# Optimization experiments

Hardware: AMD Instinct MI355X
Metric: run time of the kernel (lower is better)

The kernel has to match this reference:

```python
import jax, jax.numpy as jnp
import numpy as np

NUM_HEADS = 32
NUM_KV_HEADS = 8
HEAD_DIM = 128
HIDDEN = 4096
EPS = 1e-6
ROPE_BASE = 10000.0
NEG_INF = -1e9


def setup_inputs() -> dict:
    key = jax.random.key(0)
    ks = jax.random.split(key, 6)
    B, S = 1, 2048
    hidden_states = jax.random.normal(ks[0], (B, S, HIDDEN), dtype=jnp.float32)
    wq = jax.random.normal(ks[1], (HIDDEN, NUM_HEADS * HEAD_DIM), dtype=jnp.float32) * 0.02
    wk = jax.random.normal(ks[2], (HIDDEN, NUM_KV_HEADS * HEAD_DIM), dtype=jnp.float32) * 0.02
    wv = jax.random.normal(ks[3], (HIDDEN, NUM_KV_HEADS * HEAD_DIM), dtype=jnp.float32) * 0.02
    wo = jax.random.normal(ks[4], (NUM_HEADS * HEAD_DIM, HIDDEN), dtype=jnp.float32) * 0.02
    q_norm_w = jnp.ones((HEAD_DIM,), dtype=jnp.float32)
    k_norm_w = jnp.ones((HEAD_DIM,), dtype=jnp.float32)
    attention_mask = jnp.tril(jnp.ones((S, S), dtype=bool))[None, None]  # [1,1,S,S] causal allow-mask
    position_ids = jnp.arange(S, dtype=jnp.int64 if jax.config.jax_enable_x64 else jnp.int32)[None, :]
    return dict(hidden_states=hidden_states, wq=wq, wk=wk, wv=wv, wo=wo,
                q_norm_w=q_norm_w, k_norm_w=k_norm_w,
                attention_mask=attention_mask, position_ids=position_ids)


def _rotate_half(x):
    x1, x2 = jnp.split(x, 2, axis=-1)
    return jnp.concatenate((-x2, x1), axis=-1)


def _rms_norm(x, w):
    xf = x.astype(jnp.float32)
    var = jnp.mean(xf * xf, axis=-1, keepdims=True)
    return w * (xf * jax.lax.rsqrt(var + EPS)).astype(x.dtype)


def reference(hidden_states, wq, wk, wv, wo, q_norm_w, k_norm_w, attention_mask, position_ids):
    B, S, _ = hidden_states.shape
    dtype = hidden_states.dtype

    # projections -> [B, H, S, D]
    q = (hidden_states @ wq).reshape(B, S, NUM_HEADS, HEAD_DIM).transpose(0, 2, 1, 3)
    k = (hidden_states @ wk).reshape(B, S, NUM_KV_HEADS, HEAD_DIM).transpose(0, 2, 1, 3)
    v = (hidden_states @ wv).reshape(B, S, NUM_KV_HEADS, HEAD_DIM).transpose(0, 2, 1, 3)

    # RoPE cache (fp32), gathered by position_ids
    inv_freq = 1.0 / (ROPE_BASE ** (jnp.arange(0, HEAD_DIM, 2, dtype=jnp.float32) / HEAD_DIM))
    t = jnp.arange(S, dtype=jnp.float32)
    freqs = jnp.outer(t, inv_freq)                    # [S, D/2]
    emb = jnp.concatenate((freqs, freqs), axis=-1)    # [S, D]
    cos = jnp.cos(emb).astype(dtype)[position_ids][:, None]  # [B,1,S,D]
    sin = jnp.sin(emb).astype(dtype)[position_ids][:, None]

    q = q * cos + _rotate_half(q) * sin
    k = k * cos + _rotate_half(k) * sin

    # QK RMSNorm (after RoPE)
    q = _rms_norm(q, q_norm_w)
    k = _rms_norm(k, k_norm_w)

    # GQA repeat-kv
    n_rep = NUM_HEADS // NUM_KV_HEADS
    k = jnp.repeat(k, n_rep, axis=1)
    v = jnp.repeat(v, n_rep, axis=1)

    scores = jnp.einsum('bhqd,bhkd->bhqk', q, k) / np.sqrt(HEAD_DIM)
    scores = jnp.where(attention_mask, scores, scores + NEG_INF)
    probs = jax.nn.softmax(scores.astype(jnp.float32), axis=-1).astype(dtype)
    out = jnp.einsum('bhqk,bhkd->bhqd', probs, v)      # [B,H,S,D]
    out = out.transpose(0, 2, 1, 3).reshape(B, S, NUM_HEADS * HEAD_DIM)
    return out @ wo
```

## Files before the change

kernel.cpp:

```cpp
#include <hip/hip_runtime.h>

typedef __bf16 bf16x8 __attribute__((ext_vector_type(8)));
typedef float f32x4 __attribute__((ext_vector_type(4)));
typedef unsigned short u16x8 __attribute__((ext_vector_type(8)));
typedef unsigned short u16x4 __attribute__((ext_vector_type(4)));
typedef unsigned short u16x2 __attribute__((ext_vector_type(2)));

__device__ inline unsigned short f2bf(float f) {
    return __builtin_bit_cast(unsigned short, (__bf16)f);
}
__device__ inline float bf2f(unsigned short u) {
    return (float)__builtin_bit_cast(__bf16, u);
}

__device__ inline void storeC(float v, float* p) { *p = v; }
__device__ inline void storeC(float v, unsigned short* p) { *p = f2bf(v); }

#define MFMA16(a, b, c) __builtin_amdgcn_mfma_f32_16x16x32_bf16( \
    __builtin_bit_cast(bf16x8, a), __builtin_bit_cast(bf16x8, b), (c), 0, 0, 0)

__device__ inline void gload16(const unsigned short* g, unsigned short* l) {
    __builtin_amdgcn_global_load_lds(
        (const __attribute__((address_space(1))) unsigned int*)(g),
        (__attribute__((address_space(3))) unsigned int*)(l), 16, 0, 0);
}

__device__ __forceinline__ void bar() {
    asm volatile("" ::: "memory");
    __builtin_amdgcn_s_barrier();
    asm volatile("" ::: "memory");
}
#define WAITVM(N) asm volatile("s_waitcnt vmcnt(" #N ")" ::: "memory")

__global__ __launch_bounds__(256) void convert_f32_bf16_swz(
    const float* __restrict__ X, unsigned short* __restrict__ Y)
{
    const size_t i = ((size_t)blockIdx.x * 256 + threadIdx.x) * 8;
    const size_t row7 = (i >> 12) & 7;
    float4 v0 = *(const float4*)&X[i];
    float4 v1 = *(const float4*)&X[i + 4];
    u16x8 o;
    o[0] = f2bf(v0.x); o[1] = f2bf(v0.y); o[2] = f2bf(v0.z); o[3] = f2bf(v0.w);
    o[4] = f2bf(v1.x); o[5] = f2bf(v1.y); o[6] = f2bf(v1.z); o[7] = f2bf(v1.w);
    *(u16x8*)&Y[i ^ (row7 << 3)] = o;
}

__global__ __launch_bounds__(256) void transpose_f32_bf16(
    const float* __restrict__ W, unsigned short* __restrict__ WT, int K, int N)
{
    constexpr int LDT = 66;
    __shared__ unsigned short t_lds[64 * LDT];
    const int kt = blockIdx.x * 64, nt = blockIdx.y * 64;
    const int tid = threadIdx.x;
    const int c = (tid & 15) * 4;
    #pragma unroll
    for (int p = 0; p < 4; ++p) {
        const int r = p * 16 + (tid >> 4);
        float4 v = *(const float4*)&W[(size_t)(kt + r) * N + nt + c];
        u16x2 h0, h1;
        h0[0] = f2bf(v.x); h0[1] = f2bf(v.y);
        h1[0] = f2bf(v.z); h1[1] = f2bf(v.w);
        *(u16x2*)&t_lds[r * LDT + c] = h0;
        *(u16x2*)&t_lds[r * LDT + c + 2] = h1;
    }
    __syncthreads();
    const int kc = (tid & 7) * 8;
    #pragma unroll
    for (int p = 0; p < 2; ++p) {
        const int n = p * 32 + (tid >> 3);
        u16x8 o;
        #pragma unroll
        for (int j = 0; j < 8; ++j) o[j] = t_lds[(kc + j) * LDT + n];
        *(u16x8*)&WT[(size_t)(nt + n) * K + kt + (kc ^ ((n & 7) << 3))] = o;
    }
}

template <typename CT, int CMODE>
__global__ __launch_bounds__(512) void gemm8(
    const unsigned short* __restrict__ A, const unsigned short* __restrict__ B,
    CT* __restrict__ C, CT* __restrict__ C2, int M, int N, int K)
{
    constexpr int ASZ = 128 * 64, BSZ = 256 * 64;
    __shared__ __attribute__((aligned(16))) unsigned short a_lds[3 * ASZ];
    __shared__ __attribute__((aligned(16))) unsigned short b_lds[3 * BSZ];

    const int bm0 = blockIdx.y * 128, bn0 = blockIdx.x * 256;
    const int tid = threadIdx.x, lane = tid & 63, wid = tid >> 6;
    const int wr = wid >> 2, wc = wid & 3;
    const int l15 = lane & 15, koff = (lane >> 4) * 8;
    const int sw = (l15 & 7) << 3;
    const int cb0 = koff ^ sw;
    const int cb1 = (32 + koff) ^ sw;

    f32x4 acc[4][4] = {};

    const unsigned short* ag[2];
    const unsigned short* bg[4];
    #pragma unroll
    for (int p = 0; p < 2; ++p) {
        const int row = (wid + p * 8) * 8 + (lane >> 3);
        ag[p] = A + (size_t)(bm0 + row) * K + (lane & 7) * 8;
    }
    #pragma unroll
    for (int p = 0; p < 4; ++p) {
        const int row = (wid + p * 8) * 8 + (lane >> 3);
        bg[p] = B + (size_t)(bn0 + row) * K + (lane & 7) * 8;
    }

    const int nt = K >> 6;

    auto stageA = [&](int s, int kt, int p) {
        gload16(ag[p] + kt, a_lds + s * ASZ + (wid + p * 8) * 512);
    };
    auto stageB = [&](int s, int kt, int p) {
        gload16(bg[p] + kt, b_lds + s * BSZ + (wid + p * 8) * 512);
    };

    #pragma unroll
    for (int p = 0; p < 2; ++p) stageA(0, 0, p);
    #pragma unroll
    for (int p = 0; p < 4; ++p) stageB(0, 0, p);
    #pragma unroll
    for (int p = 0; p < 2; ++p) stageA(1, 64, p);
    #pragma unroll
    for (int p = 0; p < 4; ++p) stageB(1, 64, p);
    WAITVM(6);
    bar();

    int sc = 0;
    for (int t = 0; t < nt; ++t) {
        const unsigned short* ab = a_lds + sc * ASZ;
        const unsigned short* bb = b_lds + sc * BSZ;
        const int ss = (sc >= 1) ? sc - 1 : 2;
        const int kt2 = (t + 2) << 6;
        const bool st = (t + 2) < nt;

        u16x8 af0, af1, af2, af3, bfr[4];

        af0 = *(const u16x8*)&ab[(wr * 64 + 0 * 16 + l15) * 64 + cb0];
        af1 = *(const u16x8*)&ab[(wr * 64 + 1 * 16 + l15) * 64 + cb0];
        af2 = *(const u16x8*)&ab[(wr * 64 + 2 * 16 + l15) * 64 + cb0];
        af3 = *(const u16x8*)&ab[(wr * 64 + 3 * 16 + l15) * 64 + cb0];
        #pragma unroll
        for (int j = 0; j < 4; ++j)
            bfr[j] = *(const u16x8*)&bb[(wc * 64 + j * 16 + l15) * 64 + cb0];
        if (st) { stageA(ss, kt2, 0); stageA(ss, kt2, 1); stageB(ss, kt2, 0); }
        bar();
        __builtin_amdgcn_s_setprio(1);
        #pragma unroll
        for (int j = 0; j < 4; ++j) {
            acc[0][j] = MFMA16(af0, bfr[j], acc[0][j]);
            acc[1][j] = MFMA16(af1, bfr[j], acc[1][j]);
            acc[2][j] = MFMA16(af2, bfr[j], acc[2][j]);
            acc[3][j] = MFMA16(af3, bfr[j], acc[3][j]);
        }
        __builtin_amdgcn_s_setprio(0);

        af0 = *(const u16x8*)&ab[(wr * 64 + 0 * 16 + l15) * 64 + cb1];
        af1 = *(const u16x8*)&ab[(wr * 64 + 1 * 16 + l15) * 64 + cb1];
        af2 = *(const u16x8*)&ab[(wr * 64 + 2 * 16 + l15) * 64 + cb1];
        af3 = *(const u16x8*)&ab[(wr * 64 + 3 * 16 + l15) * 64 + cb1];
        #pragma unroll
        for (int j = 0; j < 4; ++j)
            bfr[j] = *(const u16x8*)&bb[(wc * 64 + j * 16 + l15) * 64 + cb1];
        if (st) {
            stageB(ss, kt2, 1); stageB(ss, kt2, 2); stageB(ss, kt2, 3);
            WAITVM(6);
        } else {
            WAITVM(0);
        }
        bar();
        __builtin_amdgcn_s_setprio(1);
        #pragma unroll
        for (int j = 0; j < 4; ++j) {
            acc[0][j] = MFMA16(af0, bfr[j], acc[0][j]);
            acc[1][j] = MFMA16(af1, bfr[j], acc[1][j]);
            acc[2][j] = MFMA16(af2, bfr[j], acc[2][j]);
            acc[3][j] = MFMA16(af3, bfr[j], acc[3][j]);
        }
        __builtin_amdgcn_s_setprio(0);

        bar();
        sc = (sc == 2) ? 0 : sc + 1;
    }

    #pragma unroll
    for (int i = 0; i < 4; ++i)
        #pragma unroll
        for (int r = 0; r < 4; ++r) {
            const int row = bm0 + wr * 64 + i * 16 + (lane >> 4) * 4 + r;
            if constexpr (CMODE == 0) {
                size_t base = (size_t)row * N + bn0 + wc * 64 + l15;
                #pragma unroll
                for (int j = 0; j < 4; ++j)
                    storeC(acc[i][j][r], &C[base + j * 16]);
            } else {
                #pragma unroll
                for (int j = 0; j < 4; ++j) {
                    const int col = bn0 + wc * 64 + l15 + j * 16;
                    if (col < 1024)
                        storeC(acc[i][j][r], &C[(size_t)row * 1024 + col]);
                    else
                        storeC(acc[i][j][r], &C2[(size_t)(col - 1024) * 2048 + row]);
                }
            }
        }
}

__global__ void rope_rmsnorm(unsigned short* __restrict__ X,
                             const int* __restrict__ pos_ids,
                             const float* __restrict__ W, int H, float outscale)
{
    const int s = blockIdx.x;
    const int tid = threadIdx.x;
    const int h = tid >> 3, t8 = tid & 7;
    const int rowstride = H * 128;
    unsigned short* p = X + (size_t)s * rowstride + h * 128 + t8 * 8;
    u16x8 lo = *(u16x8*)p;
    u16x8 hi = *(u16x8*)(p + 64);
    const float fpos = (float)pos_ids[s];
    float na[8], nb[8];
    float ss = 0.f;
    #pragma unroll
    for (int j = 0; j < 8; ++j) {
        const int d = t8 * 8 + j;
        float inv = expf(-0.14391156831212787f * (float)d);
        float fr = fpos * inv;
        float c = cosf(fr), sn = sinf(fr);
        float a = bf2f(lo[j]), b = bf2f(hi[j]);
        na[j] = a * c - b * sn;
        nb[j] = b * c + a * sn;
        ss += na[j] * na[j] + nb[j] * nb[j];
    }
    ss += __shfl_xor(ss, 1, 8);
    ss += __shfl_xor(ss, 2, 8);
    ss += __shfl_xor(ss, 4, 8);
    const float rn = rsqrtf(ss * (1.0f / 128.0f) + 1e-6f) * outscale;
    #pragma unroll
    for (int j = 0; j < 8; ++j) {
        const int d = t8 * 8 + j;
        lo[j] = f2bf(na[j] * rn * W[d]);
        hi[j] = f2bf(nb[j] * rn * W[d + 64]);
    }
    *(u16x8*)p = lo;
    *(u16x8*)(p + 64) = hi;
}

__global__ __launch_bounds__(256, 2) void attn_kernel(
    const unsigned short* __restrict__ Q, const unsigned short* __restrict__ K,
    const unsigned short* __restrict__ VT, unsigned short* __restrict__ O)
{
    constexpr int LDK = 136, LDV = 72, LDP = 72;
    __shared__ __attribute__((aligned(16))) unsigned short k_lds[64 * LDK];
    __shared__ __attribute__((aligned(16))) unsigned short v_lds[128 * LDV];
    __shared__ __attribute__((aligned(16))) unsigned short p_lds[4 * 32 * LDP];

    const int bid = blockIdx.x;
    const int kvh = bid & 7;
    const int rest = bid >> 3;
    const int h = kvh * 4 + (rest & 3);
    const int qb = 15 - (rest >> 2);
    const int q0 = qb * 128;
    const int tid = threadIdx.x, lane = tid & 63, wid = tid >> 6;
    const int l15 = lane & 15, g4 = (lane >> 4) * 4, koff = (lane >> 4) * 8;
    const int qw = q0 + wid * 32;

    u16x8 qf[2][4];
    #pragma unroll
    for (int qt = 0; qt < 2; ++qt)
        #pragma unroll
        for (int kk = 0; kk < 4; ++kk)
            qf[qt][kk] = *(const u16x8*)&Q[(size_t)(qw + qt * 16 + l15) * 4096 +
                                           h * 128 + kk * 32 + koff];

    f32x4 o_acc[2][8] = {};
    float m_r[2] = {-1e30f, -1e30f}, l_r[2] = {0.f, 0.f};

    const int kr = tid >> 2, kd = (tid & 3) * 32;
    const int vr = tid >> 1, vc = (tid & 1) * 32;
    const unsigned short* kg = K + (size_t)kvh * 128 + kd;
    const unsigned short* vg = VT + (size_t)(kvh * 128 + vr) * 2048 + vc;

    const int nchunk = qb * 2 + 2;
    u16x8 kst[4], vst[4];
    #pragma unroll
    for (int j = 0; j < 4; ++j) {
        kst[j] = *(const u16x8*)&kg[(size_t)kr * 1024 + j * 8];
        vst[j] = *(const u16x8*)&vg[j * 8];
    }

    for (int ch = 0; ch < nchunk; ++ch) {
        const int kv0 = ch * 64;
        __syncthreads();
        #pragma unroll
        for (int j = 0; j < 4; ++j) {
            *(u16x8*)&k_lds[kr * LDK + kd + j * 8] = kst[j];
            *(u16x8*)&v_lds[vr * LDV + vc + j * 8] = vst[j];
        }
        __syncthreads();
        if (ch + 1 < nchunk) {
            const int kv1 = kv0 + 64;
            #pragma unroll
            for (int j = 0; j < 4; ++j) {
                kst[j] = *(const u16x8*)&kg[(size_t)(kv1 + kr) * 1024 + j * 8];
                vst[j] = *(const u16x8*)&vg[kv1 + j * 8];
            }
        }

        if (kv0 <= qw + 31) {
            f32x4 sacc[2][4] = {};
            #pragma unroll
            for (int kk = 0; kk < 4; ++kk)
                #pragma unroll
                for (int jt = 0; jt < 4; ++jt) {
                    u16x8 kf = *(u16x8*)&k_lds[(jt * 16 + l15) * LDK + kk * 32 + koff];
                    #pragma unroll
                    for (int qt = 0; qt < 2; ++qt)
                        sacc[qt][jt] = MFMA16(kf, qf[qt][kk], sacc[qt][jt]);
                }

            const bool needmask = (kv0 + 63 > qw);
            #pragma unroll
            for (int qt = 0; qt < 2; ++qt) {
                const int q = qw + qt * 16 + l15;
                if (needmask) {
                    #pragma unroll
                    for (int jt = 0; jt < 4; ++jt)
                        #pragma unroll
                        for (int r = 0; r < 4; ++r)
                            if (kv0 + jt * 16 + g4 + r > q) sacc[qt][jt][r] = -1e9f;
                }
                float pmax = sacc[qt][0][0];
                #pragma unroll
                for (int jt = 0; jt < 4; ++jt)
                    #pragma unroll
                    for (int r = 0; r < 4; ++r)
                        pmax = fmaxf(pmax, sacc[qt][jt][r]);
                pmax = fmaxf(pmax, __shfl_xor(pmax, 16));
                pmax = fmaxf(pmax, __shfl_xor(pmax, 32));
                if (__any(pmax > m_r[qt] + 8.0f)) {
                    float mnew = fmaxf(m_r[qt], pmax);
                    float alpha = __expf(m_r[qt] - mnew);
                    m_r[qt] = mnew;
                    l_r[qt] *= alpha;
                    float arow[4];
                    #pragma unroll
                    for (int r = 0; r < 4; ++r)
                        arow[r] = __shfl(alpha, g4 + r, 16);
                    #pragma unroll
                    for (int nt = 0; nt < 8; ++nt)
                        #pragma unroll
                        for (int r = 0; r < 4; ++r)
                            o_acc[qt][nt][r] *= arow[r];
                }
                float ps = 0.f;
                #pragma unroll
                for (int jt = 0; jt < 4; ++jt)
                    #pragma unroll
                    for (int r = 0; r < 4; ++r) {
                        float e = __expf(sacc[qt][jt][r] - m_r[qt]);
                        sacc[qt][jt][r] = e;
                        ps += e;
                    }
                ps += __shfl_xor(ps, 16);
                ps += __shfl_xor(ps, 32);
                l_r[qt] += ps;
                const int prow = (wid * 32 + qt * 16 + l15) * LDP;
                #pragma unroll
                for (int jt = 0; jt < 4; ++jt) {
                    u16x4 w;
                    #pragma unroll
                    for (int r = 0; r < 4; ++r) w[r] = f2bf(sacc[qt][jt][r]);
                    *(u16x4*)&p_lds[prow + jt * 16 + g4] = w;
                }
            }

            u16x8 pf[2][2];
            #pragma unroll
            for (int qt = 0; qt < 2; ++qt)
                #pragma unroll
                for (int ks = 0; ks < 2; ++ks)
                    pf[qt][ks] = *(u16x8*)&p_lds[(wid * 32 + qt * 16 + l15) * LDP +
                                                 ks * 32 + koff];
            #pragma unroll
            for (int nt = 0; nt < 8; ++nt)
                #pragma unroll
                for (int ks = 0; ks < 2; ++ks) {
                    u16x8 vf = *(u16x8*)&v_lds[(nt * 16 + l15) * LDV + ks * 32 + koff];
                    #pragma unroll
                    for (int qt = 0; qt < 2; ++qt)
                        o_acc[qt][nt] = MFMA16(pf[qt][ks], vf, o_acc[qt][nt]);
                }
        }
    }

    #pragma unroll
    for (int qt = 0; qt < 2; ++qt) {
        float lrow[4];
        #pragma unroll
        for (int r = 0; r < 4; ++r)
            lrow[r] = __shfl(l_r[qt], g4 + r, 16);
        #pragma unroll
        for (int r = 0; r < 4; ++r) {
            float inv_l = 1.0f / lrow[r];
            int row = qw + qt * 16 + g4 + r;
            const int r7s = (row & 7) << 3;
            #pragma unroll
            for (int nt = 0; nt < 8; ++nt) {
                int col = h * 128 + nt * 16 + l15;
                O[(size_t)row * 4096 + (col ^ r7s)] =
                    f2bf(o_acc[qt][nt][r] * inv_l);
            }
        }
    }
}

extern "C" void kernel_launch(void* const* d_in, const int* in_sizes, int n_in,
                              void* d_out, int out_size, void* d_ws, size_t ws_size,
                              hipStream_t stream)
{
    (void)in_sizes; (void)n_in; (void)out_size; (void)ws_size;
    const float* hidden = (const float*)d_in[0];
    const float* wq     = (const float*)d_in[1];
    const float* wk     = (const float*)d_in[2];
    const float* wv     = (const float*)d_in[3];
    const float* wo     = (const float*)d_in[4];
    const float* qnw    = (const float*)d_in[5];
    const float* knw    = (const float*)d_in[6];
    const int*   pos    = (const int*)d_in[8];
    float* out = (float*)d_out;

    const size_t MB = 1024 * 1024;
    char* ws = (char*)d_ws;
    unsigned short* q_ws  = (unsigned short*)(ws);
    unsigned short* k_ws  = (unsigned short*)(ws + 16 * MB);
    unsigned short* vt_ws = (unsigned short*)(ws + 20 * MB);
    unsigned short* hb    = (unsigned short*)(ws + 24 * MB);
    unsigned short* a_ws  = hb;
    unsigned short* wqt   = (unsigned short*)(ws + 40 * MB);
    unsigned short* wkt   = (unsigned short*)(ws + 72 * MB);
    unsigned short* wvt   = (unsigned short*)(ws + 80 * MB);
    unsigned short* wot   = (unsigned short*)(ws + 88 * MB);

    convert_f32_bf16_swz<<<4096, 256, 0, stream>>>(hidden, hb);
    transpose_f32_bf16<<<dim3(64, 64), 256, 0, stream>>>(wq, wqt, 4096, 4096);
    transpose_f32_bf16<<<dim3(64, 16), 256, 0, stream>>>(wk, wkt, 4096, 1024);
    transpose_f32_bf16<<<dim3(64, 16), 256, 0, stream>>>(wv, wvt, 4096, 1024);
    transpose_f32_bf16<<<dim3(64, 64), 256, 0, stream>>>(wo, wot, 4096, 4096);

    gemm8<unsigned short, 0><<<dim3(16, 16), 512, 0, stream>>>(
        hb, wqt, q_ws, (unsigned short*)nullptr, 2048, 4096, 4096);
    gemm8<unsigned short, 2><<<dim3(8, 16), 512, 0, stream>>>(
        hb, wkt, k_ws, vt_ws, 2048, 2048, 4096);

    rope_rmsnorm<<<2048, 256, 0, stream>>>(q_ws, pos, qnw, 32, 0.08838834764831845f);
    rope_rmsnorm<<<2048, 64, 0, stream>>>(k_ws, pos, knw, 8, 1.0f);

    attn_kernel<<<512, 256, 0, stream>>>(q_ws, k_ws, vt_ws, a_ws);

    gemm8<float, 0><<<dim3(16, 16), 512, 0, stream>>>(
        a_ws, wot, out, (float*)nullptr, 2048, 4096, 4096);
}
```

Baseline: 365.7 us.

## Split-K the fused KV projection GEMM with a separate combine/transpose kernel

Result: faster. 338.2 us (-7.5%).

```diff
diff --git a/kernel.cpp b/kernel.cpp
--- a/kernel.cpp
+++ b/kernel.cpp
@@ -78,7 +78,7 @@
 template <typename CT, int CMODE>
 __global__ __launch_bounds__(512) void gemm8(
     const unsigned short* __restrict__ A, const unsigned short* __restrict__ B,
-    CT* __restrict__ C, CT* __restrict__ C2, int M, int N, int K)
+    CT* __restrict__ C, int M, int N, int K)
 {
     constexpr int ASZ = 128 * 64, BSZ = 256 * 64;
     __shared__ __attribute__((aligned(16))) unsigned short a_lds[3 * ASZ];
@@ -94,20 +94,22 @@
 
     f32x4 acc[4][4] = {};
 
+    const size_t kbase = (CMODE == 3) ? (size_t)blockIdx.z * 2048 : 0;
+
     const unsigned short* ag[2];
     const unsigned short* bg[4];
     #pragma unroll
     for (int p = 0; p < 2; ++p) {
         const int row = (wid + p * 8) * 8 + (lane >> 3);
-        ag[p] = A + (size_t)(bm0 + row) * K + (lane & 7) * 8;
+        ag[p] = A + (size_t)(bm0 + row) * K + (lane & 7) * 8 + kbase;
     }
     #pragma unroll
     for (int p = 0; p < 4; ++p) {
         const int row = (wid + p * 8) * 8 + (lane >> 3);
-        bg[p] = B + (size_t)(bn0 + row) * K + (lane & 7) * 8;
-    }
-
-    const int nt = K >> 6;
+        bg[p] = B + (size_t)(bn0 + row) * K + (lane & 7) * 8 + kbase;
+    }
+
+    const int nt = (CMODE == 3) ? 32 : (K >> 6);
 
     auto stageA = [&](int s, int kt, int p) {
         gload16(ag[p] + kt, a_lds + s * ASZ + (wid + p * 8) * 512);
@@ -184,27 +186,66 @@
         sc = (sc == 2) ? 0 : sc + 1;
     }
 
+    CT* Cb = C;
+    if constexpr (CMODE == 3)
+        Cb = C + (size_t)blockIdx.z * M * N;
+
     #pragma unroll
     for (int i = 0; i < 4; ++i)
         #pragma unroll
         for (int r = 0; r < 4; ++r) {
             const int row = bm0 + wr * 64 + i * 16 + (lane >> 4) * 4 + r;
-            if constexpr (CMODE == 0) {
-                size_t base = (size_t)row * N + bn0 + wc * 64 + l15;
-                #pragma unroll
-                for (int j = 0; j < 4; ++j)
-                    storeC(acc[i][j][r], &C[base + j * 16]);
-            } else {
-                #pragma unroll
-                for (int j = 0; j < 4; ++j) {
-                    const int col = bn0 + wc * 64 + l15 + j * 16;
-                    if (col < 1024)
-                        storeC(acc[i][j][r], &C[(size_t)row * 1024 + col]);
-                    else
-                        storeC(acc[i][j][r], &C2[(size_t)(col - 1024) * 2048 + row]);
-                }
-            }
-        }
+            size_t base = (size_t)row * N + bn0 + wc * 64 + l15;
+            #pragma unroll
+            for (int j = 0; j < 4; ++j)
+                storeC(acc[i][j][r], &Cb[base + j * 16]);
+        }
+}
+
+__global__ __launch_bounds__(256) void combine_kv(
+    const float* __restrict__ P, unsigned short* __restrict__ Kout,
+    unsigned short* __restrict__ VTout)
+{
+    const float* P0 = P;
+    const float* P1 = P + (size_t)2048 * 2048;
+    const int s0 = blockIdx.y * 64, c0 = blockIdx.x * 64;
+    const int tid = threadIdx.x;
+    const int row = tid >> 2;
+    const int cbl = (tid & 3) * 16;
+    const size_t gbase = (size_t)(s0 + row) * 2048 + c0 + cbl;
+    u16x8 o[2];
+    #pragma unroll
+    for (int j = 0; j < 2; ++j) {
+        float4 a0 = *(const float4*)&P0[gbase + j * 8];
+        float4 b0 = *(const float4*)&P1[gbase + j * 8];
+        float4 a1 = *(const float4*)&P0[gbase + j * 8 + 4];
+        float4 b1 = *(const float4*)&P1[gbase + j * 8 + 4];
+        o[j][0] = f2bf(a0.x + b0.x); o[j][1] = f2bf(a0.y + b0.y);
+        o[j][2] = f2bf(a0.z + b0.z); o[j][3] = f2bf(a0.w + b0.w);
+        o[j][4] = f2bf(a1.x + b1.x); o[j][5] = f2bf(a1.y + b1.y);
+        o[j][6] = f2bf(a1.z + b1.z); o[j][7] = f2bf(a1.w + b1.w);
+    }
+    if (c0 < 1024) {
+        #pragma unroll
+        for (int j = 0; j < 2; ++j)
+            *(u16x8*)&Kout[(size_t)(s0 + row) * 1024 + c0 + cbl + j * 8] = o[j];
+    } else {
+        constexpr int LDT = 66;
+        __shared__ unsigned short t_lds[64 * LDT];
+        #pragma unroll
+        for (int j = 0; j < 2; ++j)
+            *(u16x8*)&t_lds[row * LDT + cbl + j * 8] = o[j];
+        __syncthreads();
+        const int d = row;
+        #pragma unroll
+        for (int j = 0; j < 2; ++j) {
+            u16x8 w;
+            #pragma unroll
+            for (int e = 0; e < 8; ++e)
+                w[e] = t_lds[(cbl + j * 8 + e) * LDT + d];
+            *(u16x8*)&VTout[(size_t)(c0 - 1024 + d) * 2048 + s0 + cbl + j * 8] = w;
+        }
+    }
 }
 
 __global__ void rope_rmsnorm(unsigned short* __restrict__ X,
@@ -438,20 +479,22 @@
     unsigned short* hb    = (unsigned short*)(ws + 24 * MB);
     unsigned short* a_ws  = hb;
     unsigned short* wqt   = (unsigned short*)(ws + 40 * MB);
+    float*          kvP   = (float*)(ws + 40 * MB);
     unsigned short* wkt   = (unsigned short*)(ws + 72 * MB);
-    unsigned short* wvt   = (unsigned short*)(ws + 80 * MB);
     unsigned short* wot   = (unsigned short*)(ws + 88 * MB);
 
     convert_f32_bf16_swz<<<4096, 256, 0, stream>>>(hidden, hb);
     transpose_f32_bf16<<<dim3(64, 64), 256, 0, stream>>>(wq, wqt, 4096, 4096);
     transpose_f32_bf16<<<dim3(64, 16), 256, 0, stream>>>(wk, wkt, 4096, 1024);
-    transpose_f32_bf16<<<dim3(64, 16), 256, 0, stream>>>(wv, wvt, 4096, 1024);
+    transpose_f32_bf16<<<dim3(64, 16), 256, 0, stream>>>(
+        wv, wkt + (size_t)1024 * 4096, 4096, 1024);
     transpose_f32_bf16<<<dim3(64, 64), 256, 0, stream>>>(wo, wot, 4096, 4096);
 
     gemm8<unsigned short, 0><<<dim3(16, 16), 512, 0, stream>>>(
-        hb, wqt, q_ws, (unsigned short*)nullptr, 2048, 4096, 4096);
-    gemm8<unsigned short, 2><<<dim3(8, 16), 512, 0, stream>>>(
-        hb, wkt, k_ws, vt_ws, 2048, 2048, 4096);
+        hb, wqt, q_ws, 2048, 4096, 4096);
+    gemm8<float, 3><<<dim3(8, 16, 2), 512, 0, stream>>>(
+        hb, wkt, kvP, 2048, 2048, 4096);
+    combine_kv<<<dim3(32, 32), 256, 0, stream>>>(kvP, k_ws, vt_ws);
 
     rope_rmsnorm<<<2048, 256, 0, stream>>>(q_ws, pos, qnw, 32, 0.08838834764831845f);
     rope_rmsnorm<<<2048, 64, 0, stream>>>(k_ws, pos, knw, 8, 1.0f);
@@ -459,5 +502,5 @@
     attn_kernel<<<512, 256, 0, stream>>>(q_ws, k_ws, vt_ws, a_ws);
 
     gemm8<float, 0><<<dim3(16, 16), 512, 0, stream>>>(
-        a_ws, wot, out, (float*)nullptr, 2048, 4096, 4096);
-}
+        a_ws, wot, out, 2048, 4096, 4096);
+}
```
